# Optimization experiments

Measured on AMD Instinct MI355X. Metric: run time of the kernel, lower is better.

## Reference

```python
import math
import jax, jax.numpy as jnp
from jax import lax
import numpy as np

N, C, H, W = 32, 256, 56, 56

def setup_inputs() -> dict:
    key = jax.random.key(0)
    k = jax.random.split(key, 5)
    return {
        "x": jax.random.normal(k[0], (N, C, H, W), dtype=jnp.float32),
        "p1_w": jax.random.normal(k[1], (H, W, C, 1), dtype=jnp.float32) * 0.1,
        "conv_w": jax.random.normal(k[2], (C, C // 2, 3, 3), dtype=jnp.float32) * 0.05,
        "p4_w": jax.random.normal(k[3], (1, C, C), dtype=jnp.float32) * 0.1,
        "p5_w": jax.random.normal(k[4], (C, 1), dtype=jnp.float32) * 0.1,
    }

def reference(x, p1_w, conv_w, p4_w, p5_w):
    n, c, h, w = x.shape
    inv_sqrt_c = 1.0 / math.sqrt(c)
    # t_1: einsum 'abcd,cdef->abef' -> [n, c, c, 1] -> [n, c, c]
    t1 = jnp.einsum('nchw,hwef->ncef', x, p1_w)[..., 0]
    # t_3: grouped 3x3 conv, groups=2, no bias -> [n, c, h, w]
    t3 = lax.conv_general_dilated(
        x, conv_w, window_strides=(1, 1), padding=((1, 1), (1, 1)),
        dimension_numbers=('NCHW', 'OIHW', 'NCHW'), feature_group_count=2)
    # t_4: broadcast elementwise scale [1,c,c] * [n,c,c]
    t4 = p4_w * t1
    # t_5: [n,c,c] @ [c,1] -> [n,c]
    t5 = jnp.einsum('nab,bo->nao', t4, p5_w)[..., 0]
    # t_6: bmm(t4 [n,c,c], t3 [n,c,hw]) / sqrt(c) -> [n,c,h,w]
    t6 = (jnp.einsum('nab,nbs->nas', t4, t3.reshape(n, c, h * w))
          .reshape(n, c, h, w)) * inv_sqrt_c
    # t_7: bmm(t5 [n,1,c], x [n,c,hw]) / sqrt(c) -> [n,h,w]
    t7 = (jnp.einsum('nc,ncs->ns', t5, x.reshape(n, c, h * w))
          .reshape(n, h, w)) * inv_sqrt_c
    # t_8: broadcast add [n,1,h,w] + [n,c,h,w]
    return t7[:, None, :, :] + t6
```

## Files before the change

kernel.cpp:

```cpp
#include <hip/hip_runtime.h>

#define HWB   3136
#define HWPAD 3200
#define SPAD  3364

typedef __attribute__((ext_vector_type(8))) short bf16x8;
typedef __attribute__((ext_vector_type(4))) float f32x4;

__device__ __forceinline__ unsigned short f2bf(float f) {
    unsigned u = __float_as_uint(f);
    unsigned r = (u + 0x7fffu + ((u >> 16) & 1u)) >> 16;
    return (unsigned short)r;
}
__device__ __forceinline__ float bf2f(unsigned short h) {
    return __uint_as_float(((unsigned)h) << 16);
}
__device__ __forceinline__ void gl_lds16(const void* g, void* l) {
    __builtin_amdgcn_global_load_lds(
        (const __attribute__((address_space(1))) void*)g,
        (__attribute__((address_space(3))) void*)l, 16, 0, 0);
}

__global__ __launch_bounds__(256) void k_prep(
    const float* __restrict__ x, unsigned short* __restrict__ xc,
    unsigned short* __restrict__ xp)
{
    __shared__ unsigned short tile[32][33];
    const int n = blockIdx.z, c0 = blockIdx.y * 32, s0 = blockIdx.x * 32;
    const int lx = threadIdx.x & 31, ly = threadIdx.x >> 5;
    const float* xb = x + ((size_t)(n * 256 + c0)) * HWB + s0;
    unsigned short* xcb = xc + ((size_t)(n * 256 + c0)) * HWB + s0;
#pragma unroll
    for (int it = 0; it < 4; ++it) {
        int lc = ly + it * 8;
        unsigned short b = f2bf(xb[(size_t)lc * HWB + lx]);
        tile[lc][lx] = b;
        xcb[(size_t)lc * HWB + lx] = b;
    }
    __syncthreads();
    unsigned short* ob = xp + (size_t)n * SPAD * 256 + c0;
#pragma unroll
    for (int it = 0; it < 4; ++it) {
        int ls = ly + it * 8;
        int s = s0 + ls;
        int sp = s + 2 * (s / 56) + 59;
        ob[(size_t)sp * 256 + lx] = tile[lx][ls];
    }
}

__global__ __launch_bounds__(256) void k_prep_p1t(
    const float* __restrict__ p1, unsigned short* __restrict__ p1t)
{
    __shared__ unsigned short tile[32][33];
    const int e0 = blockIdx.y * 32, h0 = blockIdx.x * 32;
    const int lx = threadIdx.x & 31, ly = threadIdx.x >> 5;
#pragma unroll
    for (int it = 0; it < 4; ++it) {
        int lh = ly + it * 8;
        tile[lh][lx] = f2bf(p1[(size_t)(h0 + lh) * 256 + e0 + lx]);
    }
    __syncthreads();
#pragma unroll
    for (int it = 0; it < 4; ++it) {
        int le = ly + it * 8;
        p1t[(size_t)(e0 + le) * HWB + h0 + lx] = tile[lx][le];
    }
}

__global__ __launch_bounds__(256) void k_prep_w(
    const float* __restrict__ w, unsigned short* __restrict__ wp,
    unsigned short* __restrict__ xp)
{
    const int o = blockIdx.x, t = threadIdx.x;
#pragma unroll
    for (int k = t; k < 1152; k += 256) {
        int tap = k >> 7, ci = k & 127;
        wp[(size_t)o * 1152 + k] = f2bf(w[(size_t)o * 1152 + ci * 9 + tap]);
    }
    if (o < 32) {
        unsigned short* xpn = xp + (size_t)o * SPAD * 256;
        for (int sp = t; sp < SPAD; sp += 256) {
            int y = sp / 58, xcol = sp - y * 58;
            if (y == 0 || y == 57 || xcol == 0 || xcol == 57) {
                ushort4 z4 = {0, 0, 0, 0};
#pragma unroll
                for (int k = 0; k < 64; ++k)
                    *(ushort4*)&xpn[(size_t)sp * 256 + k * 4] = z4;
            }
        }
    }
}

__global__ __launch_bounds__(256) void k_conv(
    const unsigned short* __restrict__ xp, const unsigned short* __restrict__ wp,
    unsigned short* __restrict__ t3cl)
{
    __shared__ short As[128 * 64];
    __shared__ short Bs[128 * 64];
    const int tid = threadIdx.x;
    const int n = blockIdx.y >> 1, g = blockIdx.y & 1;
    const int tileS = blockIdx.x * 128;
    const int wave = tid >> 6, lane = tid & 63;
    const int wm = (wave >> 1) * 64, wn = (wave & 1) * 64;

    const int rl = tid >> 3, q = tid & 7;
    const int swq = (q ^ (rl & 7)) * 8;

    const unsigned short* xpn = xp + (size_t)n * SPAD * 256 + g * 128 + swq;
    const unsigned short* arow[4];
    const unsigned short* brow[4];
#pragma unroll
    for (int p = 0; p < 4; ++p) {
        int s = tileS + p * 32 + rl;
        int sc = s < HWB ? s : HWB - 1;
        int sp = sc + 2 * (sc / 56) + 59;
        arow[p] = xpn + (size_t)sp * 256;
        brow[p] = wp + (size_t)(g * 128 + p * 32 + rl) * 1152 + swq;
    }

    f32x4 acc[4][4] = {};
    const int frow = lane & 15, quad = lane >> 4, sw = frow & 7;
    int rofA[4], rofB[4];
#pragma unroll
    for (int i = 0; i < 4; ++i) {
        rofA[i] = (wm + i * 16 + frow) * 64;
        rofB[i] = (wn + i * 16 + frow) * 64;
    }

#pragma unroll
    for (int t = 0; t < 18; ++t) {
        const int tap = t >> 1;
        const int shift = ((tap / 3 - 1) * 58 + (tap % 3 - 1)) * 256 + (t & 1) * 64;
        __syncthreads();
#pragma unroll
        for (int p = 0; p < 4; ++p) {
            gl_lds16(arow[p] + shift, &As[(p * 32 + rl) * 64 + q * 8]);
            gl_lds16(brow[p] + t * 64, &Bs[(p * 32 + rl) * 64 + q * 8]);
        }
        __syncthreads();
#pragma unroll
        for (int h = 0; h < 2; ++h) {
            bf16x8 af[4], bfr[4];
#pragma unroll
            for (int i = 0; i < 4; ++i)
                af[i] = *(const bf16x8*)&As[rofA[i] + ((h * 4 + quad) ^ sw) * 8];
#pragma unroll
            for (int j = 0; j < 4; ++j)
                bfr[j] = *(const bf16x8*)&Bs[rofB[j] + ((h * 4 + quad) ^ sw) * 8];
#pragma unroll
            for (int i = 0; i < 4; ++i)
#pragma unroll
                for (int j = 0; j < 4; ++j)
                    acc[i][j] = __builtin_amdgcn_mfma_f32_16x16x32_bf16(af[i], bfr[j], acc[i][j], 0, 0, 0);
        }
    }
    unsigned short* ob = t3cl + (size_t)n * HWPAD * 256 + g * 128;
#pragma unroll
    for (int i = 0; i < 4; ++i)
#pragma unroll
        for (int r = 0; r < 4; ++r) {
            int s = tileS + wm + i * 16 + (lane >> 4) * 4 + r;
            int c = wn + (lane & 15);
#pragma unroll
            for (int j = 0; j < 4; ++j) {
                float v = (s < HWB) ? acc[i][j][r] : 0.f;
                ob[(size_t)s * 256 + c + j * 16] = f2bf(v);
            }
        }
}

__global__ __launch_bounds__(256) void k_gemm1(
    const unsigned short* __restrict__ xc, const unsigned short* __restrict__ p1t,
    float* __restrict__ part)
{
    __shared__ short As[128 * 64];
    __shared__ short Bs[128 * 64];
    const int tid = threadIdx.x;
    const int z = blockIdx.z;
    const int tileM = blockIdx.y * 128;
    const int tileN = blockIdx.x * 128;
    const int kbase = z ? (832 + (z - 1) * 768) : 0;
    const int nk = z ? 12 : 13;
    const int wave = tid >> 6, lane = tid & 63;
    const int wm = (wave >> 1) * 64, wn = (wave & 1) * 64;

    const int rl = tid >> 3, q = tid & 7;
    const int swq = (q ^ (rl & 7)) * 8;
    const unsigned short* asrc = xc + (size_t)(tileM + rl) * HWB + kbase + swq;
    const unsigned short* bsrc = p1t + (size_t)(tileN + rl) * HWB + kbase + swq;

    f32x4 acc[4][4] = {};
    const int frow = lane & 15, quad = lane >> 4, sw = frow & 7;

    for (int k0 = 0; k0 < nk * 64; k0 += 64) {
        __syncthreads();
#pragma unroll
        for (int p = 0; p < 4; ++p) {
            gl_lds16(asrc + (size_t)(p * 32) * HWB + k0, &As[(p * 32 + rl) * 64 + q * 8]);
            gl_lds16(bsrc + (size_t)(p * 32) * HWB + k0, &Bs[(p * 32 + rl) * 64 + q * 8]);
        }
        __syncthreads();
#pragma unroll
        for (int h = 0; h < 2; ++h) {
            bf16x8 af[4], bfr[4];
#pragma unroll
            for (int i = 0; i < 4; ++i)
                af[i] = *(const bf16x8*)&As[(wm + i * 16 + frow) * 64 + ((h * 4 + quad) ^ sw) * 8];
#pragma unroll
            for (int j = 0; j < 4; ++j)
                bfr[j] = *(const bf16x8*)&Bs[(wn + j * 16 + frow) * 64 + ((h * 4 + quad) ^ sw) * 8];
#pragma unroll
            for (int i = 0; i < 4; ++i)
#pragma unroll
                for (int j = 0; j < 4; ++j)
                    acc[i][j] = __builtin_amdgcn_mfma_f32_16x16x32_bf16(af[i], bfr[j], acc[i][j], 0, 0, 0);
        }
    }
    float* ob = part + (size_t)z * 8192 * 256;
#pragma unroll
    for (int j = 0; j < 4; ++j) {
        const int e = tileN + wn + j * 16 + (lane & 15);
#pragma unroll
        for (int i = 0; i < 4; ++i)
#pragma unroll
            for (int r = 0; r < 4; ++r) {
                int m = tileM + wm + i * 16 + (lane >> 4) * 4 + r;
                ob[(size_t)m * 256 + e] = acc[i][j][r];
            }
    }
}

__global__ __launch_bounds__(256) void k_t4scale(
    const float* __restrict__ part, const float* __restrict__ p4,
    const float* __restrict__ p5, unsigned short* __restrict__ t4h,
    float* __restrict__ t5)
{
    const int row = blockIdx.x * 4 + (threadIdx.x >> 6);
    const int lane = threadIdx.x & 63;
    const size_t off = (size_t)row * 256 + lane * 4;
    const size_t slab = (size_t)8192 * 256;
    float4 a0 = *(const float4*)&part[off];
    float4 a1 = *(const float4*)&part[off + slab];
    float4 a2 = *(const float4*)&part[off + 2 * slab];
    float4 a3 = *(const float4*)&part[off + 3 * slab];
    float4 a;
    a.x = (a0.x + a1.x) + (a2.x + a3.x);
    a.y = (a0.y + a1.y) + (a2.y + a3.y);
    a.z = (a0.z + a1.z) + (a2.z + a3.z);
    a.w = (a0.w + a1.w) + (a2.w + a3.w);
    float4 sc = *(const float4*)&p4[(size_t)(row & 255) * 256 + lane * 4];
    float4 pv = *(const float4*)&p5[lane * 4];
    float v0 = a.x * sc.x, v1 = a.y * sc.y, v2 = a.z * sc.z, v3 = a.w * sc.w;
    ushort4 o;
    o.x = f2bf(v0); o.y = f2bf(v1); o.z = f2bf(v2); o.w = f2bf(v3);
    *(ushort4*)&t4h[(size_t)row * 256 + lane * 4] = o;
    float sum = v0 * pv.x + v1 * pv.y + v2 * pv.z + v3 * pv.w;
#pragma unroll
    for (int offd = 32; offd > 0; offd >>= 1) sum += __shfl_down(sum, offd);
    if (lane == 0) t5[row] = sum;
}

__global__ __launch_bounds__(256) void k_t7(
    const unsigned short* __restrict__ xp, const float* __restrict__ t5,
    float* __restrict__ t7)
{
    const int n = blockIdx.y;
    const int wave = threadIdx.x >> 6, lane = threadIdx.x & 63;
    float4 w = *(const float4*)&t5[n * 256 + lane * 4];
    const int s0 = blockIdx.x * 16 + wave * 4;
#pragma unroll
    for (int qq = 0; qq < 4; ++qq) {
        const int s = s0 + qq;
        const int sp = s + 2 * (s / 56) + 59;
        ushort4 a = *(const ushort4*)&xp[((size_t)n * SPAD + sp) * 256 + lane * 4];
        float sum = bf2f(a.x) * w.x + bf2f(a.y) * w.y + bf2f(a.z) * w.z + bf2f(a.w) * w.w;
#pragma unroll
        for (int off = 32; off > 0; off >>= 1) sum += __shfl_down(sum, off);
        if (lane == 0) t7[n * HWB + s] = sum * 0.0625f;
    }
}

__global__ __launch_bounds__(256) void k_bmm(
    const unsigned short* __restrict__ t4h, const unsigned short* __restrict__ t3cl,
    const float* __restrict__ t7, float* __restrict__ out)
{
    __shared__ short As[128 * 64];
    __shared__ short Bs[128 * 64];
    const int tid = threadIdx.x;
    const int n = blockIdx.z;
    const int tileA = blockIdx.y * 128;
    const int tileS = blockIdx.x * 128;
    const int wave = tid >> 6, lane = tid & 63;
    const int wm = (wave >> 1) * 64, wn = (wave & 1) * 64;

    const int rl = tid >> 3, q = tid & 7;
    const int swq = (q ^ (rl & 7)) * 8;
    const unsigned short* asrc = t4h + ((size_t)n * 256 + tileA + rl) * 256 + swq;
    const unsigned short* bsrc = t3cl + ((size_t)n * HWPAD + tileS + rl) * 256 + swq;

    f32x4 acc[4][4] = {};
    const int frow = lane & 15, quad = lane >> 4, sw = frow & 7;

    for (int k0 = 0; k0 < 256; k0 += 64) {
        __syncthreads();
#pragma unroll
        for (int p = 0; p < 4; ++p) {
            gl_lds16(asrc + (size_t)(p * 32) * 256 + k0, &As[(p * 32 + rl) * 64 + q * 8]);
            gl_lds16(bsrc + (size_t)(p * 32) * 256 + k0, &Bs[(p * 32 + rl) * 64 + q * 8]);
        }
        __syncthreads();
#pragma unroll
        for (int h = 0; h < 2; ++h) {
            bf16x8 af[4], bfr[4];
#pragma unroll
            for (int i = 0; i < 4; ++i)
                af[i] = *(const bf16x8*)&As[(wm + i * 16 + frow) * 64 + ((h * 4 + quad) ^ sw) * 8];
#pragma unroll
            for (int j = 0; j < 4; ++j)
                bfr[j] = *(const bf16x8*)&Bs[(wn + j * 16 + frow) * 64 + ((h * 4 + quad) ^ sw) * 8];
#pragma unroll
            for (int i = 0; i < 4; ++i)
#pragma unroll
                for (int j = 0; j < 4; ++j)
                    acc[i][j] = __builtin_amdgcn_mfma_f32_16x16x32_bf16(af[i], bfr[j], acc[i][j], 0, 0, 0);
        }
    }
    const float* t7n = t7 + (size_t)n * HWB;
    float* ob = out + (size_t)n * 256 * HWB;
#pragma unroll
    for (int j = 0; j < 4; ++j) {
        int s = tileS + wn + j * 16 + (lane & 15);
        bool vsx = s < HWB;
        float t7v = vsx ? t7n[s] : 0.f;
        if (!vsx) continue;
#pragma unroll
        for (int i = 0; i < 4; ++i)
#pragma unroll
            for (int r = 0; r < 4; ++r) {
                int a = tileA + wm + i * 16 + (lane >> 4) * 4 + r;
                ob[(size_t)a * HWB + s] = acc[i][j][r] * 0.0625f + t7v;
            }
    }
}

extern "C" void kernel_launch(void* const* d_in, const int* in_sizes, int n_in,
                              void* d_out, int out_size, void* d_ws, size_t ws_size,
                              hipStream_t stream) {
    const float* x  = (const float*)d_in[0];
    const float* p1 = (const float*)d_in[1];
    const float* cw = (const float*)d_in[2];
    const float* p4 = (const float*)d_in[3];
    const float* p5 = (const float*)d_in[4];

    char* w = (char*)d_ws;
    unsigned short* xp    = (unsigned short*)w;  w += (size_t)32 * SPAD * 256 * 2;
    unsigned short* t3cl  = (unsigned short*)w;  w += (size_t)32 * HWPAD * 256 * 2;
    unsigned short* p1t   = (unsigned short*)w;  w += (size_t)256 * HWB * 2;
    unsigned short* wpack = (unsigned short*)w;  w += (size_t)256 * 1152 * 2;
    unsigned short* t4h   = (unsigned short*)w;  w += (size_t)8192 * 256 * 2;
    float* t5             = (float*)w;           w += (size_t)8192 * 4;
    float* t7             = (float*)w;           w += (size_t)32 * HWB * 4;

    char* o = (char*)d_out;
    unsigned short* xc = (unsigned short*)o;
    float* part        = (float*)(o + (size_t)32 * 256 * HWB * 2);
    float* out = (float*)d_out;

    k_prep    <<<dim3(98, 8, 32), 256, 0, stream>>>(x, xc, xp);
    k_prep_p1t<<<dim3(98, 8),     256, 0, stream>>>(p1, p1t);
    k_prep_w  <<<dim3(256),       256, 0, stream>>>(cw, wpack, xp);
    k_conv    <<<dim3(25, 64),    256, 0, stream>>>(xp, wpack, t3cl);
    k_gemm1   <<<dim3(2, 64, 4),  256, 0, stream>>>(xc, p1t, part);
    k_t4scale <<<dim3(2048),      256, 0, stream>>>(part, p4, p5, t4h, t5);
    k_t7      <<<dim3(196, 32),   256, 0, stream>>>(xp, t5, t7);
    k_bmm     <<<dim3(25, 2, 32), 256, 0, stream>>>(t4h, t3cl, t7, out);
}
```

Before: 370.1 us.

## Double-buffer LDS tiles and remap workgroups by XCD in GEMM kernels

The three MFMA GEMM kernels (conv, gemm1, bmm) now use two LDS buffers. The loads for the next K step are issued before the current step's MFMAs, with one barrier per iteration instead of two, so global-to-LDS latency overlaps with compute. Launch grids are flattened to 1D, and block ids are remapped so consecutive tiles sharing inputs land on the same XCD, which should improve L2 reuse. LDS use per block doubles to 64KB, which may lower occupancy.

```diff
diff --git a/kernel.cpp b/kernel.cpp
--- a/kernel.cpp
+++ b/kernel.cpp
@@ -95,11 +95,14 @@
     const unsigned short* __restrict__ xp, const unsigned short* __restrict__ wp,
     unsigned short* __restrict__ t3cl)
 {
-    __shared__ short As[128 * 64];
-    __shared__ short Bs[128 * 64];
+    __shared__ short As[2][128 * 64];
+    __shared__ short Bs[2][128 * 64];
     const int tid = threadIdx.x;
-    const int n = blockIdx.y >> 1, g = blockIdx.y & 1;
-    const int tileS = blockIdx.x * 128;
+    const int orig = blockIdx.x;
+    const int wgid = (orig & 7) * 200 + (orig >> 3);
+    const int ng = wgid / 25;
+    const int tileS = (wgid - ng * 25) * 128;
+    const int n = ng >> 1, g = ng & 1;
     const int wave = tid >> 6, lane = tid & 63;
     const int wm = (wave >> 1) * 64, wn = (wave & 1) * 64;
 
@@ -126,33 +129,50 @@
         rofA[i] = (wm + i * 16 + frow) * 64;
         rofB[i] = (wn + i * 16 + frow) * 64;
     }
-
+    const int ldst = (tid >> 3) * 64 + (tid & 7) * 8;
+
+    {
+        const int shift0 = (-59) * 256;
+#pragma unroll
+        for (int p = 0; p < 4; ++p) {
+            gl_lds16(arow[p] + shift0, &As[0][p * 2048 + ldst]);
+            gl_lds16(brow[p], &Bs[0][p * 2048 + ldst]);
+        }
+    }
+    __syncthreads();
+
+    int cur = 0;
 #pragma unroll
     for (int t = 0; t < 18; ++t) {
-        const int tap = t >> 1;
-        const int shift = ((tap / 3 - 1) * 58 + (tap % 3 - 1)) * 256 + (t & 1) * 64;
-        __syncthreads();
-#pragma unroll
-        for (int p = 0; p < 4; ++p) {
-            gl_lds16(arow[p] + shift, &As[(p * 32 + rl) * 64 + q * 8]);
-            gl_lds16(brow[p] + t * 64, &Bs[(p * 32 + rl) * 64 + q * 8]);
-        }
-        __syncthreads();
+        if (t < 17) {
+            const int tn = t + 1;
+            const int tap = tn >> 1;
+            const int shift = ((tap / 3 - 1) * 58 + (tap % 3 - 1)) * 256 + (tn & 1) * 64;
+#pragma unroll
+            for (int p = 0; p < 4; ++p) {
+                gl_lds16(arow[p] + shift, &As[cur ^ 1][p * 2048 + ldst]);
+                gl_lds16(brow[p] + tn * 64, &Bs[cur ^ 1][p * 2048 + ldst]);
+            }
+        }
+        const short* Ab = As[cur];
+        const short* Bb = Bs[cur];
 #pragma unroll
         for (int h = 0; h < 2; ++h) {
             bf16x8 af[4], bfr[4];
 #pragma unroll
             for (int i = 0; i < 4; ++i)
-                af[i] = *(const bf16x8*)&As[rofA[i] + ((h * 4 + quad) ^ sw) * 8];
+                af[i] = *(const bf16x8*)&Ab[rofA[i] + ((h * 4 + quad) ^ sw) * 8];
 #pragma unroll
             for (int j = 0; j < 4; ++j)
-                bfr[j] = *(const bf16x8*)&Bs[rofB[j] + ((h * 4 + quad) ^ sw) * 8];
+                bfr[j] = *(const bf16x8*)&Bb[rofB[j] + ((h * 4 + quad) ^ sw) * 8];
 #pragma unroll
             for (int i = 0; i < 4; ++i)
 #pragma unroll
                 for (int j = 0; j < 4; ++j)
                     acc[i][j] = __builtin_amdgcn_mfma_f32_16x16x32_bf16(af[i], bfr[j], acc[i][j], 0, 0, 0);
         }
+        __syncthreads();
+        cur ^= 1;
     }
     unsigned short* ob = t3cl + (size_t)n * HWPAD * 256 + g * 128;
 #pragma unroll
@@ -173,12 +193,15 @@
     const unsigned short* __restrict__ xc, const unsigned short* __restrict__ p1t,
     float* __restrict__ part)
 {
-    __shared__ short As[128 * 64];
-    __shared__ short Bs[128 * 64];
+    __shared__ short As[2][128 * 64];
+    __shared__ short Bs[2][128 * 64];
     const int tid = threadIdx.x;
-    const int z = blockIdx.z;
-    const int tileM = blockIdx.y * 128;
-    const int tileN = blockIdx.x * 128;
+    const int orig = blockIdx.x;
+    const int wgid = (orig & 7) * 64 + (orig >> 3);
+    const int z = wgid >> 7;
+    const int rem = wgid & 127;
+    const int tileM = (rem >> 1) * 128;
+    const int tileN = (rem & 1) * 128;
     const int kbase = z ? (832 + (z - 1) * 768) : 0;
     const int nk = z ? 12 : 13;
     const int wave = tid >> 6, lane = tid & 63;
@@ -191,30 +214,44 @@
 
     f32x4 acc[4][4] = {};
     const int frow = lane & 15, quad = lane >> 4, sw = frow & 7;
-
-    for (int k0 = 0; k0 < nk * 64; k0 += 64) {
-        __syncthreads();
-#pragma unroll
-        for (int p = 0; p < 4; ++p) {
-            gl_lds16(asrc + (size_t)(p * 32) * HWB + k0, &As[(p * 32 + rl) * 64 + q * 8]);
-            gl_lds16(bsrc + (size_t)(p * 32) * HWB + k0, &Bs[(p * 32 + rl) * 64 + q * 8]);
-        }
-        __syncthreads();
+    const int ldst = rl * 64 + q * 8;
+
+#pragma unroll
+    for (int p = 0; p < 4; ++p) {
+        gl_lds16(asrc + (size_t)(p * 32) * HWB, &As[0][p * 2048 + ldst]);
+        gl_lds16(bsrc + (size_t)(p * 32) * HWB, &Bs[0][p * 2048 + ldst]);
+    }
+    __syncthreads();
+
+    int cur = 0;
+    for (int i2 = 0; i2 < nk; ++i2) {
+        if (i2 + 1 < nk) {
+            const int kn = (i2 + 1) * 64;
+#pragma unroll
+            for (int p = 0; p < 4; ++p) {
+                gl_lds16(asrc + (size_t)(p * 32) * HWB + kn, &As[cur ^ 1][p * 2048 + ldst]);
+                gl_lds16(bsrc + (size_t)(p * 32) * HWB + kn, &Bs[cur ^ 1][p * 2048 + ldst]);
+            }
+        }
+        const short* Ab = As[cur];
+        const short* Bb = Bs[cur];
 #pragma unroll
         for (int h = 0; h < 2; ++h) {
             bf16x8 af[4], bfr[4];
 #pragma unroll
             for (int i = 0; i < 4; ++i)
-                af[i] = *(const bf16x8*)&As[(wm + i * 16 + frow) * 64 + ((h * 4 + quad) ^ sw) * 8];
+                af[i] = *(const bf16x8*)&Ab[(wm + i * 16 + frow) * 64 + ((h * 4 + quad) ^ sw) * 8];
 #pragma unroll
             for (int j = 0; j < 4; ++j)
-                bfr[j] = *(const bf16x8*)&Bs[(wn + j * 16 + frow) * 64 + ((h * 4 + quad) ^ sw) * 8];
+                bfr[j] = *(const bf16x8*)&Bb[(wn + j * 16 + frow) * 64 + ((h * 4 + quad) ^ sw) * 8];
 #pragma unroll
             for (int i = 0; i < 4; ++i)
 #pragma unroll
                 for (int j = 0; j < 4; ++j)
                     acc[i][j] = __builtin_amdgcn_mfma_f32_16x16x32_bf16(af[i], bfr[j], acc[i][j], 0, 0, 0);
         }
+        __syncthreads();
+        cur ^= 1;
     }
     float* ob = part + (size_t)z * 8192 * 256;
 #pragma unroll
@@ -284,12 +321,15 @@
     const unsigned short* __restrict__ t4h, const unsigned short* __restrict__ t3cl,
     const float* __restrict__ t7, float* __restrict__ out)
 {
-    __shared__ short As[128 * 64];
-    __shared__ short Bs[128 * 64];
+    __shared__ short As[2][128 * 64];
+    __shared__ short Bs[2][128 * 64];
     const int tid = threadIdx.x;
-    const int n = blockIdx.z;
-    const int tileA = blockIdx.y * 128;
-    const int tileS = blockIdx.x * 128;
+    const int orig = blockIdx.x;
+    const int wgid = (orig & 7) * 200 + (orig >> 3);
+    const int n = wgid / 50;
+    const int rem = wgid - n * 50;
+    const int tileA = (rem / 25) * 128;
+    const int tileS = (rem % 25) * 128;
     const int wave = tid >> 6, lane = tid & 63;
     const int wm = (wave >> 1) * 64, wn = (wave & 1) * 64;
 
@@ -300,30 +340,45 @@
 
     f32x4 acc[4][4] = {};
     const int frow = lane & 15, quad = lane >> 4, sw = frow & 7;
-
+    const int ldst = rl * 64 + q * 8;
+
+#pragma unroll
+    for (int p = 0; p < 4; ++p) {
+        gl_lds16(asrc + (size_t)(p * 32) * 256, &As[0][p * 2048 + ldst]);
+        gl_lds16(bsrc + (size_t)(p * 32) * 256, &Bs[0][p * 2048 + ldst]);
+    }
+    __syncthreads();
+
+    int cur = 0;
+#pragma unroll
     for (int k0 = 0; k0 < 256; k0 += 64) {
-        __syncthreads();
-#pragma unroll
-        for (int p = 0; p < 4; ++p) {
-            gl_lds16(asrc + (size_t)(p * 32) * 256 + k0, &As[(p * 32 + rl) * 64 + q * 8]);
-            gl_lds16(bsrc + (size_t)(p * 32) * 256 + k0, &Bs[(p * 32 + rl) * 64 + q * 8]);
-        }
-        __syncthreads();
+        if (k0 < 192) {
+            const int kn = k0 + 64;
+#pragma unroll
+            for (int p = 0; p < 4; ++p) {
+                gl_lds16(asrc + (size_t)(p * 32) * 256 + kn, &As[cur ^ 1][p * 2048 + ldst]);
+                gl_lds16(bsrc + (size_t)(p * 32) * 256 + kn, &Bs[cur ^ 1][p * 2048 + ldst]);
+            }
+        }
+        const short* Ab = As[cur];
+        const short* Bb = Bs[cur];
 #pragma unroll
         for (int h = 0; h < 2; ++h) {
             bf16x8 af[4], bfr[4];
 #pragma unroll
             for (int i = 0; i < 4; ++i)
-                af[i] = *(const bf16x8*)&As[(wm + i * 16 + frow) * 64 + ((h * 4 + quad) ^ sw) * 8];
+                af[i] = *(const bf16x8*)&Ab[(wm + i * 16 + frow) * 64 + ((h * 4 + quad) ^ sw) * 8];
 #pragma unroll
             for (int j = 0; j < 4; ++j)
-                bfr[j] = *(const bf16x8*)&Bs[(wn + j * 16 + frow) * 64 + ((h * 4 + quad) ^ sw) * 8];
+                bfr[j] = *(const bf16x8*)&Bb[(wn + j * 16 + frow) * 64 + ((h * 4 + quad) ^ sw) * 8];
 #pragma unroll
             for (int i = 0; i < 4; ++i)
 #pragma unroll
                 for (int j = 0; j < 4; ++j)
                     acc[i][j] = __builtin_amdgcn_mfma_f32_16x16x32_bf16(af[i], bfr[j], acc[i][j], 0, 0, 0);
         }
+        __syncthreads();
+        cur ^= 1;
     }
     const float* t7n = t7 + (size_t)n * HWB;
     float* ob = out + (size_t)n * 256 * HWB;
@@ -369,9 +424,9 @@
     k_prep    <<<dim3(98, 8, 32), 256, 0, stream>>>(x, xc, xp);
     k_prep_p1t<<<dim3(98, 8),     256, 0, stream>>>(p1, p1t);
     k_prep_w  <<<dim3(256),       256, 0, stream>>>(cw, wpack, xp);
-    k_conv    <<<dim3(25, 64),    256, 0, stream>>>(xp, wpack, t3cl);
-    k_gemm1   <<<dim3(2, 64, 4),  256, 0, stream>>>(xc, p1t, part);
+    k_conv    <<<dim3(1600),      256, 0, stream>>>(xp, wpack, t3cl);
+    k_gemm1   <<<dim3(512),       256, 0, stream>>>(xc, p1t, part);
     k_t4scale <<<dim3(2048),      256, 0, stream>>>(part, p4, p5, t4h, t5);
     k_t7      <<<dim3(196, 32),   256, 0, stream>>>(xp, t5, t7);
-    k_bmm     <<<dim3(25, 2, 32), 256, 0, stream>>>(t4h, t3cl, t7, out);
-}
+    k_bmm     <<<dim3(1600),      256, 0, stream>>>(t4h, t3cl, t7, out);
+}
```

After: 368.5 us. About the same (-0.4%).
